# Optimization experiments

Measured on AMD Instinct MI355X. Metric: run time of the kernel, lower is better.

The kernel has to match this reference:

```python
import jax, jax.numpy as jnp
import numpy as np

B, T, D = 1, 2048, 2048
NH, NKV, HD = 16, 4, 128
REP = NH // NKV
ROPE_BASE = 10000.0


def rms_norm(x):
    # matches F.rms_norm default eps = finfo(dtype).eps
    eps = jnp.asarray(jnp.finfo(x.dtype).eps, x.dtype)
    return x * jax.lax.rsqrt(jnp.mean(x * x, axis=-1, keepdims=True) + eps)


def apply_rope(x, cos, sin):
    h = x.shape[-1] // 2
    x1, x2 = x[..., :h], x[..., h:]
    return jnp.concatenate([x1 * cos + x2 * sin, -x1 * sin + x2 * cos], axis=-1)


def setup_inputs() -> dict:
    key = jax.random.key(0)
    ks = jax.random.split(key, 9)
    s = 0.02  # weight init scale
    return {
        "x": jax.random.normal(ks[0], (B, T, D), jnp.float32),
        "skip": jax.random.normal(ks[1], (B, T, D), jnp.float32),
        "wq": jax.random.normal(ks[2], (D, D), jnp.float32) * s,
        "wk": jax.random.normal(ks[3], (NKV * HD, D), jnp.float32) * s,
        "wv": jax.random.normal(ks[4], (NKV * HD, D), jnp.float32) * s,
        "wproj": jax.random.normal(ks[5], (D, D), jnp.float32) * s,
        "qk_g": jnp.ones((NH,), jnp.float32),  # qk_init**0.5 with qk_init=1.0
        "ln_s": jnp.ones((1,), jnp.float32),
        "v_bias": jax.random.normal(ks[6], (NKV, HD), jnp.float32) * 0.01,
    }


def reference(x, skip, wq, wk, wv, wproj, qk_g, ln_s, v_bias):
    Bc, Tc, Dc = x.shape
    q = (x @ wq.T).reshape(Bc, Tc, NH, HD)        # [B,T,NH,HD]
    k = (x @ wk.T).reshape(Bc, Tc, NKV, HD)       # [B,T,NKV,HD]
    v = (x @ wv.T).reshape(Bc, Tc, NKV, HD) + v_bias[None, None, :, :]

    # skip-gate blend
    g = jax.nn.sigmoid(ln_s * 0.1)                # [1]
    ks_ = (skip @ wk.T).reshape(Bc, Tc, NKV, HD)
    vs_ = (skip @ wv.T).reshape(Bc, Tc, NKV, HD)
    k = k * (1.0 - g) + ks_ * g
    v = v * (1.0 - g) + vs_ * g

    q = rms_norm(q)
    k = rms_norm(k)

    # RoPE tables: [1, T, 1, HD/2]
    t = jnp.arange(Tc, dtype=jnp.float32)
    inv_freq = 1.0 / (ROPE_BASE ** (jnp.arange(0, HD, 2, dtype=jnp.float32) / HD))
    fr = t[:, None] * inv_freq[None, :]
    cos = jnp.cos(fr)[None, :, None, :].astype(x.dtype)
    sin = jnp.sin(fr)[None, :, None, :].astype(x.dtype)
    q = apply_rope(q, cos, sin)
    k = apply_rope(k, cos, sin)

    # per-head gain on q and on repeated k (effective gain^2 on logits)
    gain = jnp.abs(qk_g).astype(x.dtype)          # [NH]
    q = q * gain[None, None, :, None]
    k = jnp.repeat(k, REP, axis=2) * gain[None, None, :, None]  # [B,T,NH,HD]
    v = jnp.repeat(v, REP, axis=2)                               # [B,T,NH,HD]

    scale = 1.0 / jnp.sqrt(jnp.asarray(HD, x.dtype))
    scores = jnp.einsum('bqhd,bkhd->bhqk', q, k) * scale         # [B,NH,T,T]
    causal = jnp.tril(jnp.ones((Tc, Tc), dtype=bool))
    scores = jnp.where(causal[None, None], scores, -jnp.inf)
    attn = jax.nn.softmax(scores, axis=-1)
    y = jnp.einsum('bhqk,bkhd->bqhd', attn, v).reshape(Bc, Tc, Dc)
    return (y @ wproj.T) * ln_s.astype(x.dtype)
```

## Files before the change

### kernel.cpp

```cpp
#include <hip/hip_runtime.h>


typedef float  f32x4 __attribute__((ext_vector_type(4)));
typedef short  s16x8 __attribute__((ext_vector_type(8)));
typedef unsigned short u16;

#define DEVI __device__ __forceinline__

DEVI u16 f2bf(float f) {
  union { float f; unsigned u; } c; c.f = f;
  unsigned u = c.u + 0x7fffu + ((c.u >> 16) & 1u);
  return (u16)(u >> 16);
}

DEVI void gl_lds16(const void* g, void* l) {
  __builtin_amdgcn_global_load_lds(
      (const __attribute__((address_space(1))) unsigned int*)g,
      (__attribute__((address_space(3))) unsigned int*)l, 16, 0, 0);
}

__global__ __launch_bounds__(256) void prep_kernel(
    const float* __restrict__ x, const float* __restrict__ skip,
    const float* __restrict__ ln_s, const float* __restrict__ v_bias,
    u16* __restrict__ xb, u16* __restrict__ xmb, float* __restrict__ colbias) {
  float g = 1.0f / (1.0f + __expf(-ln_s[0] * 0.1f));
  int i = (blockIdx.x * 256 + threadIdx.x) * 4;
  float4 xv = *(const float4*)(x + i);
  float4 sv = *(const float4*)(skip + i);
  ushort4 a, b;
  a.x = f2bf(xv.x); a.y = f2bf(xv.y); a.z = f2bf(xv.z); a.w = f2bf(xv.w);
  b.x = f2bf((1.f - g) * xv.x + g * sv.x);
  b.y = f2bf((1.f - g) * xv.y + g * sv.y);
  b.z = f2bf((1.f - g) * xv.z + g * sv.z);
  b.w = f2bf((1.f - g) * xv.w + g * sv.w);
  *(ushort4*)(xb + i) = a;
  *(ushort4*)(xmb + i) = b;
  if (blockIdx.x == 0) {
    int t = threadIdx.x;
    for (int k = t; k < 512; k += 256) {
      colbias[k] = 0.f;
      colbias[512 + k] = (1.f - g) * v_bias[k];
    }
  }
}

__global__ __launch_bounds__(256) void convw_kernel(
    const float* __restrict__ wq, const float* __restrict__ wk,
    const float* __restrict__ wv, const float* __restrict__ wp,
    u16* __restrict__ wb) {
  size_t i = ((size_t)blockIdx.x * 256 + threadIdx.x) * 4;
  constexpr size_t M4 = 4u * 1024 * 1024, M1 = 1024 * 1024;
  const float* src;
  if (i < M4) src = wq + i;
  else if (i < M4 + M1) src = wk + (i - M4);
  else if (i < M4 + 2 * M1) src = wv + (i - M4 - M1);
  else src = wp + (i - M4 - 2 * M1);
  float4 v = *(const float4*)src;
  ushort4 o;
  o.x = f2bf(v.x); o.y = f2bf(v.y); o.z = f2bf(v.z); o.w = f2bf(v.w);
  *(ushort4*)(wb + i) = o;
}

template <int BIAS, int SCALE>
__global__ __launch_bounds__(256) void gemm_nt(
    const u16* __restrict__ A, const u16* __restrict__ B, float* __restrict__ C,
    int M, int N, int K, const float* __restrict__ bias,
    const float* __restrict__ scale) {
  __shared__ u16 lA[128 * 32];
  __shared__ u16 lB[128 * 32];
  const int tid = threadIdx.x;
  const int lane = tid & 63, w = tid >> 6;
  const int m0 = blockIdx.y * 128, n0 = blockIdx.x * 128;
  const int mo = (w >> 1) * 64, no = (w & 1) * 64;
  const int r16 = lane & 15, q4 = lane >> 4;
  f32x4 acc[4][4] = {};

  for (int k0 = 0; k0 < K; k0 += 32) {
#pragma unroll
    for (int j = 0; j < 2; ++j) {
      int slot = j * 256 + tid;
      int row = slot >> 2, c8 = (slot & 3) * 8;
      gl_lds16(A + (size_t)(m0 + row) * K + k0 + c8, &lA[slot * 8]);
    }
#pragma unroll
    for (int j = 0; j < 2; ++j) {
      int slot = j * 256 + tid;
      int row = slot >> 2, c8 = (slot & 3) * 8;
      gl_lds16(B + (size_t)(n0 + row) * K + k0 + c8, &lB[slot * 8]);
    }
    __syncthreads();
    s16x8 af[4], bfr[4];
#pragma unroll
    for (int i = 0; i < 4; ++i)
      af[i] = *(const s16x8*)&lA[(mo + i * 16 + r16) * 32 + q4 * 8];
#pragma unroll
    for (int i = 0; i < 4; ++i)
      bfr[i] = *(const s16x8*)&lB[(no + i * 16 + r16) * 32 + q4 * 8];
#pragma unroll
    for (int mi = 0; mi < 4; ++mi)
#pragma unroll
      for (int ni = 0; ni < 4; ++ni)
        acc[mi][ni] = __builtin_amdgcn_mfma_f32_16x16x32_bf16(
            af[mi], bfr[ni], acc[mi][ni], 0, 0, 0);
    __syncthreads();
  }
  float sc = SCALE ? scale[0] : 1.0f;
#pragma unroll
  for (int mi = 0; mi < 4; ++mi) {
#pragma unroll
    for (int ni = 0; ni < 4; ++ni) {
      int col = n0 + no + ni * 16 + r16;
      float bv = BIAS ? bias[col] : 0.0f;
#pragma unroll
      for (int r = 0; r < 4; ++r) {
        int row = m0 + mo + mi * 16 + q4 * 4 + r;
        C[(size_t)row * N + col] = (acc[mi][ni][r] + bv) * sc;
      }
    }
  }
}

__global__ __launch_bounds__(256) void postqk_kernel(
    const float* __restrict__ qraw, const float* __restrict__ kvraw,
    const float* __restrict__ qk_g, u16* __restrict__ qb,
    u16* __restrict__ kb) {
  constexpr int T = 2048;
  const int lane = threadIdx.x & 63, w = threadIdx.x >> 6;
  int p = blockIdx.x * 4 + w;
  const float* src;
  u16* dst;
  int t;
  float extra = 1.0f;
  if (p < 16 * T) {
    int hh = p >> 11; t = p & 2047;
    src = qraw + (size_t)t * 2048 + hh * 128;
    dst = qb + ((size_t)hh * T + t) * 128;
    float g = qk_g[hh];
    extra = g * g * 0.12751742f;
  } else {
    p -= 16 * T;
    int hh = p >> 11; t = p & 2047;
    src = kvraw + (size_t)t * 1024 + hh * 128;
    dst = kb + ((size_t)hh * T + t) * 128;
  }
  float x1 = src[lane], x2 = src[lane + 64];
  float ss = x1 * x1 + x2 * x2;
  ss += __shfl_xor(ss, 1);  ss += __shfl_xor(ss, 2);  ss += __shfl_xor(ss, 4);
  ss += __shfl_xor(ss, 8);  ss += __shfl_xor(ss, 16); ss += __shfl_xor(ss, 32);
  float rn = rsqrtf(ss * (1.0f / 128.0f) + 1.1920929e-7f) * extra;
  float fr = (float)t * expf((float)lane * -0.14391156831212787f);
  float c = cosf(fr), s = sinf(fr);
  float y1 = (x1 * c + x2 * s) * rn;
  float y2 = (x2 * c - x1 * s) * rn;
  dst[lane] = f2bf(y1);
  dst[lane + 64] = f2bf(y2);
}

__global__ __launch_bounds__(256) void transv_kernel(
    const float* __restrict__ kvraw, u16* __restrict__ vT) {
  constexpr int T = 2048;
  __shared__ float tile[32][33];
  int t0 = blockIdx.x * 32, hd0 = blockIdx.y * 32;
  int tx = threadIdx.x & 31, ty = threadIdx.x >> 5;
#pragma unroll
  for (int i = 0; i < 4; ++i) {
    int t = t0 + ty + i * 8;
    tile[ty + i * 8][tx] = kvraw[(size_t)t * 1024 + 512 + hd0 + tx];
  }
  __syncthreads();
#pragma unroll
  for (int i = 0; i < 4; ++i) {
    int hd = hd0 + ty + i * 8;
    vT[(size_t)hd * T + t0 + tx] = f2bf(tile[tx][ty + i * 8]);
  }
}

__global__ __launch_bounds__(256) void flash_kernel(
    const u16* __restrict__ qb, const u16* __restrict__ kb,
    const u16* __restrict__ vT, u16* __restrict__ out) {
  constexpr int T = 2048;
  __shared__ u16 lK[2][64 * 128];
  __shared__ u16 lV[2][128 * 64];
  __shared__ u16 lP[4][16 * 72];
  const int tid = threadIdx.x, lane = tid & 63, w = tid >> 6;
  const int h = blockIdx.y, hkv = h >> 2;
  const int q0 = (int)(gridDim.x - 1 - blockIdx.x) * 64;
  const int r16 = lane & 15, q4 = lane >> 4;
  const int qrow = q0 + w * 16 + q4 * 4;

  s16x8 qf[4];
  {
    const u16* qp = qb + ((size_t)h * T + q0 + w * 16 + r16) * 128 + q4 * 8;
#pragma unroll
    for (int d = 0; d < 4; ++d) qf[d] = *(const s16x8*)(qp + d * 32);
  }

  const u16* kbase = kb + (size_t)hkv * T * 128;
  const u16* vbase = vT + (size_t)hkv * 128 * T;
  int ks_off[4], vs_off[4];
#pragma unroll
  for (int j = 0; j < 4; ++j) {
    int slot = j * 256 + tid;
    int krow = slot >> 4, kc = slot & 15;
    int kcb = (kc * 16) ^ ((krow & 7) << 4);
    ks_off[j] = krow * 128 + (kcb >> 1);
    int vrow = slot >> 3, vc = slot & 7;
    int vcb = (vc * 16) ^ ((vrow & 7) << 4);
    vs_off[j] = vrow * T + (vcb >> 1);
  }

  f32x4 O[8] = {};
  float m_[4], l_[4];
#pragma unroll
  for (int r = 0; r < 4; ++r) { m_[r] = -3.0e38f; l_[r] = 0.f; }
  const int nt = q0 / 64 + 1;

#pragma unroll
  for (int j = 0; j < 4; ++j)
    gl_lds16(kbase + ks_off[j], &lK[0][(j * 256 + tid) * 8]);
#pragma unroll
  for (int j = 0; j < 4; ++j)
    gl_lds16(vbase + vs_off[j], &lV[0][(j * 256 + tid) * 8]);
  asm volatile("s_waitcnt vmcnt(0)" ::: "memory");
  __builtin_amdgcn_s_barrier();

  for (int it = 0; it < nt; ++it) {
    const int t0 = it * 64;
    const int cur = it & 1;
    if (it + 1 < nt) {
      const int nxt = (it + 1) * 64;
#pragma unroll
      for (int j = 0; j < 4; ++j)
        gl_lds16(kbase + (size_t)nxt * 128 + ks_off[j],
                 &lK[cur ^ 1][(j * 256 + tid) * 8]);
#pragma unroll
      for (int j = 0; j < 4; ++j)
        gl_lds16(vbase + nxt + vs_off[j],
                 &lV[cur ^ 1][(j * 256 + tid) * 8]);
    }
    const u16* Kt = lK[cur];
    const u16* Vt = lV[cur];

    f32x4 s[4];
#pragma unroll
    for (int kvh = 0; kvh < 4; ++kvh) {
      f32x4 acc = {};
#pragma unroll
      for (int d = 0; d < 4; ++d) {
        int cb = ((q4 * 16 + d * 64) ^ ((r16 & 7) << 4)) >> 1;
        acc = __builtin_amdgcn_mfma_f32_16x16x32_bf16(
            qf[d], *(const s16x8*)(Kt + (kvh * 16 + r16) * 128 + cb), acc, 0, 0, 0);
      }
      s[kvh] = acc;
    }

    if (t0 + 64 > q0 + w * 16) {
#pragma unroll
      for (int kvh = 0; kvh < 4; ++kvh)
#pragma unroll
        for (int r = 0; r < 4; ++r)
          s[kvh][r] = (t0 + kvh * 16 + r16 <= qrow + r) ? s[kvh][r] : -1.0e30f;
    }

    float al[4];
#pragma unroll
    for (int r = 0; r < 4; ++r) {
      float t = fmaxf(fmaxf(s[0][r], s[1][r]), fmaxf(s[2][r], s[3][r]));
      t = fmaxf(t, __shfl_xor(t, 1));
      t = fmaxf(t, __shfl_xor(t, 2));
      t = fmaxf(t, __shfl_xor(t, 4));
      t = fmaxf(t, __shfl_xor(t, 8));
      float mn = fmaxf(m_[r], t);
      al[r] = __builtin_amdgcn_exp2f(m_[r] - mn);
      m_[r] = mn;
    }
    u16* myP = lP[w];
#pragma unroll
    for (int r = 0; r < 4; ++r) {
      float ps = 0.f;
      int prow = (q4 * 4 + r) * 72;
#pragma unroll
      for (int kvh = 0; kvh < 4; ++kvh) {
        float pp = __builtin_amdgcn_exp2f(s[kvh][r] - m_[r]);
        myP[prow + kvh * 16 + r16] = f2bf(pp);
        ps += pp;
      }
      ps += __shfl_xor(ps, 1); ps += __shfl_xor(ps, 2);
      ps += __shfl_xor(ps, 4); ps += __shfl_xor(ps, 8);
      l_[r] = l_[r] * al[r] + ps;
    }
#pragma unroll
    for (int dt = 0; dt < 8; ++dt)
#pragma unroll
      for (int r = 0; r < 4; ++r) O[dt][r] *= al[r];

    asm volatile("s_waitcnt lgkmcnt(0)" ::: "memory");
    __builtin_amdgcn_sched_barrier(0);
    s16x8 pf0 = *(const s16x8*)&myP[r16 * 72 + q4 * 8];
    s16x8 pf1 = *(const s16x8*)&myP[r16 * 72 + 32 + q4 * 8];

    int cb0 = ((q4 * 16) ^ ((r16 & 7) << 4)) >> 1;
    int cb1 = ((64 + q4 * 16) ^ ((r16 & 7) << 4)) >> 1;
#pragma unroll
    for (int dt = 0; dt < 8; ++dt) {
      const u16* vr = Vt + (dt * 16 + r16) * 64;
      O[dt] = __builtin_amdgcn_mfma_f32_16x16x32_bf16(
          pf0, *(const s16x8*)(vr + cb0), O[dt], 0, 0, 0);
      O[dt] = __builtin_amdgcn_mfma_f32_16x16x32_bf16(
          pf1, *(const s16x8*)(vr + cb1), O[dt], 0, 0, 0);
    }

    asm volatile("s_waitcnt vmcnt(0)" ::: "memory");
    __builtin_amdgcn_s_barrier();
  }

  float inv[4];
#pragma unroll
  for (int r = 0; r < 4; ++r) inv[r] = 1.0f / l_[r];
#pragma unroll
  for (int dt = 0; dt < 8; ++dt) {
#pragma unroll
    for (int r = 0; r < 4; ++r) {
      int row = qrow + r;
      int col = h * 128 + dt * 16 + r16;
      out[(size_t)row * 2048 + col] = f2bf(O[dt][r] * inv[r]);
    }
  }
}

extern "C" void kernel_launch(void* const* d_in, const int* in_sizes, int n_in,
                              void* d_out, int out_size, void* d_ws,
                              size_t ws_size, hipStream_t stream) {
  const float* x      = (const float*)d_in[0];
  const float* skip   = (const float*)d_in[1];
  const float* wq     = (const float*)d_in[2];
  const float* wk     = (const float*)d_in[3];
  const float* wv     = (const float*)d_in[4];
  const float* wp     = (const float*)d_in[5];
  const float* qk_g   = (const float*)d_in[6];
  const float* ln_s   = (const float*)d_in[7];
  const float* v_bias = (const float*)d_in[8];
  float* out = (float*)d_out;

  constexpr size_t MB = 1024 * 1024;
  char* ws = (char*)d_ws;
  u16*   wb    = (u16*)(ws);
  u16*   xb    = (u16*)(ws + 20 * MB);
  u16*   xmb   = (u16*)(ws + 28 * MB);
  float* qraw  = (float*)(ws + 36 * MB);
  float* kvraw = (float*)(ws + 52 * MB);
  u16*   qb    = (u16*)(ws + 60 * MB);
  u16*   kb    = (u16*)(ws + 68 * MB);
  u16*   vT    = (u16*)(ws + 70 * MB);
  u16*   ao    = (u16*)(ws + 72 * MB);
  float* colbias = (float*)(ws + 80 * MB);

  prep_kernel<<<4096, 256, 0, stream>>>(x, skip, ln_s, v_bias, xb, xmb,
                                        colbias);
  convw_kernel<<<10240, 256, 0, stream>>>(wq, wk, wv, wp, wb);
  gemm_nt<0, 0><<<dim3(16, 16), 256, 0, stream>>>(xb, wb, qraw, 2048, 2048,
                                                  2048, nullptr, nullptr);
  gemm_nt<1, 0><<<dim3(8, 16), 256, 0, stream>>>(
      xmb, wb + 4 * MB, kvraw, 2048, 1024, 2048, colbias, nullptr);
  postqk_kernel<<<10240, 256, 0, stream>>>(qraw, kvraw, qk_g, qb, kb);
  transv_kernel<<<dim3(64, 16), 256, 0, stream>>>(kvraw, vT);
  flash_kernel<<<dim3(32, 16), 256, 0, stream>>>(qb, kb, vT, ao);
  gemm_nt<0, 1><<<dim3(16, 16), 256, 0, stream>>>(
      ao, wb + 6 * MB, out, 2048, 2048, 2048, nullptr, ln_s);
}
```

Measured before the change: 354.7 us.

## Split-K GEMMs with bf16 partials and single-wave flash blocks reading K/V from global

The three GEMMs now split K across blockIdx.z and write bf16 partial sums. The consumers (postqk, transv, and a new reduce_out kernel) add the partials back together, and the reduce kernel also applies the ln_s scale. This raises block counts on a GPU with many CUs. The flash kernel becomes one wave per block (16 query rows) and loads K and V straight from global memory instead of double-buffering them through LDS, so there are far more blocks but no shared K/V reuse. Storing partials in bf16 loses some precision, and the extra reduction pass adds memory traffic.

```diff
diff --git a/kernel.cpp b/kernel.cpp
--- a/kernel.cpp
+++ b/kernel.cpp
@@ -11,6 +11,10 @@
   union { float f; unsigned u; } c; c.f = f;
   unsigned u = c.u + 0x7fffu + ((c.u >> 16) & 1u);
   return (u16)(u >> 16);
+}
+DEVI float bf2f(u16 v) {
+  union { unsigned u; float f; } c; c.u = ((unsigned)v) << 16;
+  return c.f;
 }
 
 DEVI void gl_lds16(const void* g, void* l) {
@@ -61,21 +65,22 @@
   *(ushort4*)(wb + i) = o;
 }
 
-template <int BIAS, int SCALE>
-__global__ __launch_bounds__(256) void gemm_nt(
-    const u16* __restrict__ A, const u16* __restrict__ B, float* __restrict__ C,
-    int M, int N, int K, const float* __restrict__ bias,
-    const float* __restrict__ scale) {
+template <int BIAS>
+__global__ __launch_bounds__(256) void gemm_sk(
+    const u16* __restrict__ A, const u16* __restrict__ B, u16* __restrict__ Cp,
+    int M, int N, int KS, int K, const float* __restrict__ bias) {
   __shared__ u16 lA[128 * 32];
   __shared__ u16 lB[128 * 32];
   const int tid = threadIdx.x;
   const int lane = tid & 63, w = tid >> 6;
   const int m0 = blockIdx.y * 128, n0 = blockIdx.x * 128;
+  const int z = blockIdx.z;
   const int mo = (w >> 1) * 64, no = (w & 1) * 64;
   const int r16 = lane & 15, q4 = lane >> 4;
+  const int kbeg = z * KS;
   f32x4 acc[4][4] = {};
 
-  for (int k0 = 0; k0 < K; k0 += 32) {
+  for (int k0 = kbeg; k0 < kbeg + KS; k0 += 32) {
 #pragma unroll
     for (int j = 0; j < 2; ++j) {
       int slot = j * 256 + tid;
@@ -104,46 +109,52 @@
             af[mi], bfr[ni], acc[mi][ni], 0, 0, 0);
     __syncthreads();
   }
-  float sc = SCALE ? scale[0] : 1.0f;
+  u16* Cz = Cp + (size_t)z * M * N;
 #pragma unroll
   for (int mi = 0; mi < 4; ++mi) {
 #pragma unroll
     for (int ni = 0; ni < 4; ++ni) {
       int col = n0 + no + ni * 16 + r16;
-      float bv = BIAS ? bias[col] : 0.0f;
+      float bv = (BIAS && z == 0) ? bias[col] : 0.0f;
 #pragma unroll
       for (int r = 0; r < 4; ++r) {
         int row = m0 + mo + mi * 16 + q4 * 4 + r;
-        C[(size_t)row * N + col] = (acc[mi][ni][r] + bv) * sc;
+        Cz[(size_t)row * N + col] = f2bf(acc[mi][ni][r] + bv);
       }
     }
   }
 }
 
 __global__ __launch_bounds__(256) void postqk_kernel(
-    const float* __restrict__ qraw, const float* __restrict__ kvraw,
+    const u16* __restrict__ qrawp, const u16* __restrict__ kvrawp,
     const float* __restrict__ qk_g, u16* __restrict__ qb,
     u16* __restrict__ kb) {
   constexpr int T = 2048;
+  constexpr size_t QPS = (size_t)T * 2048;
+  constexpr size_t KPS = (size_t)T * 1024;
   const int lane = threadIdx.x & 63, w = threadIdx.x >> 6;
   int p = blockIdx.x * 4 + w;
-  const float* src;
   u16* dst;
   int t;
-  float extra = 1.0f;
+  float x1, x2, extra = 1.0f;
   if (p < 16 * T) {
     int hh = p >> 11; t = p & 2047;
-    src = qraw + (size_t)t * 2048 + hh * 128;
+    const u16* s0 = qrawp + (size_t)t * 2048 + hh * 128;
+    x1 = bf2f(s0[lane]) + bf2f(s0[QPS + lane]);
+    x2 = bf2f(s0[lane + 64]) + bf2f(s0[QPS + lane + 64]);
     dst = qb + ((size_t)hh * T + t) * 128;
     float g = qk_g[hh];
     extra = g * g * 0.12751742f;
   } else {
     p -= 16 * T;
     int hh = p >> 11; t = p & 2047;
-    src = kvraw + (size_t)t * 1024 + hh * 128;
+    const u16* s0 = kvrawp + (size_t)t * 1024 + hh * 128;
+    x1 = bf2f(s0[lane]) + bf2f(s0[KPS + lane]) + bf2f(s0[2 * KPS + lane]) +
+         bf2f(s0[3 * KPS + lane]);
+    x2 = bf2f(s0[lane + 64]) + bf2f(s0[KPS + lane + 64]) +
+         bf2f(s0[2 * KPS + lane + 64]) + bf2f(s0[3 * KPS + lane + 64]);
     dst = kb + ((size_t)hh * T + t) * 128;
   }
-  float x1 = src[lane], x2 = src[lane + 64];
   float ss = x1 * x1 + x2 * x2;
   ss += __shfl_xor(ss, 1);  ss += __shfl_xor(ss, 2);  ss += __shfl_xor(ss, 4);
   ss += __shfl_xor(ss, 8);  ss += __shfl_xor(ss, 16); ss += __shfl_xor(ss, 32);
@@ -157,15 +168,18 @@
 }
 
 __global__ __launch_bounds__(256) void transv_kernel(
-    const float* __restrict__ kvraw, u16* __restrict__ vT) {
+    const u16* __restrict__ kvrawp, u16* __restrict__ vT) {
   constexpr int T = 2048;
+  constexpr size_t KPS = (size_t)T * 1024;
   __shared__ float tile[32][33];
   int t0 = blockIdx.x * 32, hd0 = blockIdx.y * 32;
   int tx = threadIdx.x & 31, ty = threadIdx.x >> 5;
 #pragma unroll
   for (int i = 0; i < 4; ++i) {
     int t = t0 + ty + i * 8;
-    tile[ty + i * 8][tx] = kvraw[(size_t)t * 1024 + 512 + hd0 + tx];
+    const u16* s0 = kvrawp + (size_t)t * 1024 + 512 + hd0 + tx;
+    tile[ty + i * 8][tx] =
+        bf2f(s0[0]) + bf2f(s0[KPS]) + bf2f(s0[2 * KPS]) + bf2f(s0[3 * KPS]);
   }
   __syncthreads();
 #pragma unroll
@@ -175,93 +189,60 @@
   }
 }
 
-__global__ __launch_bounds__(256) void flash_kernel(
+__global__ __launch_bounds__(64) void flash_kernel(
     const u16* __restrict__ qb, const u16* __restrict__ kb,
     const u16* __restrict__ vT, u16* __restrict__ out) {
   constexpr int T = 2048;
-  __shared__ u16 lK[2][64 * 128];
-  __shared__ u16 lV[2][128 * 64];
-  __shared__ u16 lP[4][16 * 72];
-  const int tid = threadIdx.x, lane = tid & 63, w = tid >> 6;
+  __shared__ u16 lP[16 * 72];
+  const int lane = threadIdx.x;
   const int h = blockIdx.y, hkv = h >> 2;
-  const int q0 = (int)(gridDim.x - 1 - blockIdx.x) * 64;
+  const int qt = (int)(gridDim.x - 1 - blockIdx.x);
+  const int q0w = qt * 16;
   const int r16 = lane & 15, q4 = lane >> 4;
-  const int qrow = q0 + w * 16 + q4 * 4;
+  const int qrow = q0w + q4 * 4;
 
   s16x8 qf[4];
   {
-    const u16* qp = qb + ((size_t)h * T + q0 + w * 16 + r16) * 128 + q4 * 8;
+    const u16* qp = qb + ((size_t)h * T + q0w + r16) * 128 + q4 * 8;
 #pragma unroll
     for (int d = 0; d < 4; ++d) qf[d] = *(const s16x8*)(qp + d * 32);
   }
-
   const u16* kbase = kb + (size_t)hkv * T * 128;
   const u16* vbase = vT + (size_t)hkv * 128 * T;
-  int ks_off[4], vs_off[4];
-#pragma unroll
-  for (int j = 0; j < 4; ++j) {
-    int slot = j * 256 + tid;
-    int krow = slot >> 4, kc = slot & 15;
-    int kcb = (kc * 16) ^ ((krow & 7) << 4);
-    ks_off[j] = krow * 128 + (kcb >> 1);
-    int vrow = slot >> 3, vc = slot & 7;
-    int vcb = (vc * 16) ^ ((vrow & 7) << 4);
-    vs_off[j] = vrow * T + (vcb >> 1);
-  }
 
   f32x4 O[8] = {};
   float m_[4], l_[4];
 #pragma unroll
   for (int r = 0; r < 4; ++r) { m_[r] = -3.0e38f; l_[r] = 0.f; }
-  const int nt = q0 / 64 + 1;
-
-#pragma unroll
-  for (int j = 0; j < 4; ++j)
-    gl_lds16(kbase + ks_off[j], &lK[0][(j * 256 + tid) * 8]);
-#pragma unroll
-  for (int j = 0; j < 4; ++j)
-    gl_lds16(vbase + vs_off[j], &lV[0][(j * 256 + tid) * 8]);
-  asm volatile("s_waitcnt vmcnt(0)" ::: "memory");
-  __builtin_amdgcn_s_barrier();
+  const int nt = q0w / 64 + 1;
 
   for (int it = 0; it < nt; ++it) {
     const int t0 = it * 64;
-    const int cur = it & 1;
-    if (it + 1 < nt) {
-      const int nxt = (it + 1) * 64;
-#pragma unroll
-      for (int j = 0; j < 4; ++j)
-        gl_lds16(kbase + (size_t)nxt * 128 + ks_off[j],
-                 &lK[cur ^ 1][(j * 256 + tid) * 8]);
-#pragma unroll
-      for (int j = 0; j < 4; ++j)
-        gl_lds16(vbase + nxt + vs_off[j],
-                 &lV[cur ^ 1][(j * 256 + tid) * 8]);
-    }
-    const u16* Kt = lK[cur];
-    const u16* Vt = lV[cur];
-
     f32x4 s[4];
+    const u16* kt = kbase + (size_t)t0 * 128 + q4 * 8;
 #pragma unroll
     for (int kvh = 0; kvh < 4; ++kvh) {
+      const u16* kr = kt + (kvh * 16 + r16) * 128;
       f32x4 acc = {};
-#pragma unroll
-      for (int d = 0; d < 4; ++d) {
-        int cb = ((q4 * 16 + d * 64) ^ ((r16 & 7) << 4)) >> 1;
-        acc = __builtin_amdgcn_mfma_f32_16x16x32_bf16(
-            qf[d], *(const s16x8*)(Kt + (kvh * 16 + r16) * 128 + cb), acc, 0, 0, 0);
-      }
+      acc = __builtin_amdgcn_mfma_f32_16x16x32_bf16(qf[0], *(const s16x8*)(kr), acc, 0, 0, 0);
+      acc = __builtin_amdgcn_mfma_f32_16x16x32_bf16(qf[1], *(const s16x8*)(kr + 32), acc, 0, 0, 0);
+      acc = __builtin_amdgcn_mfma_f32_16x16x32_bf16(qf[2], *(const s16x8*)(kr + 64), acc, 0, 0, 0);
+      acc = __builtin_amdgcn_mfma_f32_16x16x32_bf16(qf[3], *(const s16x8*)(kr + 96), acc, 0, 0, 0);
       s[kvh] = acc;
     }
-
-    if (t0 + 64 > q0 + w * 16) {
+    const u16* vt = vbase + t0 + q4 * 8;
+    s16x8 vf[8];
+#pragma unroll
+    for (int dt = 0; dt < 8; ++dt)
+      vf[dt] = *(const s16x8*)(vt + (size_t)(dt * 16 + r16) * T);
+
+    if (t0 + 64 > q0w) {
 #pragma unroll
       for (int kvh = 0; kvh < 4; ++kvh)
 #pragma unroll
         for (int r = 0; r < 4; ++r)
           s[kvh][r] = (t0 + kvh * 16 + r16 <= qrow + r) ? s[kvh][r] : -1.0e30f;
     }
-
     float al[4];
 #pragma unroll
     for (int r = 0; r < 4; ++r) {
@@ -274,7 +255,6 @@
       al[r] = __builtin_amdgcn_exp2f(m_[r] - mn);
       m_[r] = mn;
     }
-    u16* myP = lP[w];
 #pragma unroll
     for (int r = 0; r < 4; ++r) {
       float ps = 0.f;
@@ -282,7 +262,7 @@
 #pragma unroll
       for (int kvh = 0; kvh < 4; ++kvh) {
         float pp = __builtin_amdgcn_exp2f(s[kvh][r] - m_[r]);
-        myP[prow + kvh * 16 + r16] = f2bf(pp);
+        lP[prow + kvh * 16 + r16] = f2bf(pp);
         ps += pp;
       }
       ps += __shfl_xor(ps, 1); ps += __shfl_xor(ps, 2);
@@ -296,22 +276,18 @@
 
     asm volatile("s_waitcnt lgkmcnt(0)" ::: "memory");
     __builtin_amdgcn_sched_barrier(0);
-    s16x8 pf0 = *(const s16x8*)&myP[r16 * 72 + q4 * 8];
-    s16x8 pf1 = *(const s16x8*)&myP[r16 * 72 + 32 + q4 * 8];
-
-    int cb0 = ((q4 * 16) ^ ((r16 & 7) << 4)) >> 1;
-    int cb1 = ((64 + q4 * 16) ^ ((r16 & 7) << 4)) >> 1;
-#pragma unroll
-    for (int dt = 0; dt < 8; ++dt) {
-      const u16* vr = Vt + (dt * 16 + r16) * 64;
-      O[dt] = __builtin_amdgcn_mfma_f32_16x16x32_bf16(
-          pf0, *(const s16x8*)(vr + cb0), O[dt], 0, 0, 0);
-      O[dt] = __builtin_amdgcn_mfma_f32_16x16x32_bf16(
-          pf1, *(const s16x8*)(vr + cb1), O[dt], 0, 0, 0);
-    }
-
-    asm volatile("s_waitcnt vmcnt(0)" ::: "memory");
-    __builtin_amdgcn_s_barrier();
+    s16x8 pf0 = *(const s16x8*)&lP[r16 * 72 + q4 * 8];
+    s16x8 pf1 = *(const s16x8*)&lP[r16 * 72 + 32 + q4 * 8];
+
+#pragma unroll
+    for (int dt = 0; dt < 8; ++dt)
+      O[dt] = __builtin_amdgcn_mfma_f32_16x16x32_bf16(pf0, vf[dt], O[dt], 0, 0, 0);
+#pragma unroll
+    for (int dt = 0; dt < 8; ++dt)
+      vf[dt] = *(const s16x8*)(vt + 32 + (size_t)(dt * 16 + r16) * T);
+#pragma unroll
+    for (int dt = 0; dt < 8; ++dt)
+      O[dt] = __builtin_amdgcn_mfma_f32_16x16x32_bf16(pf1, vf[dt], O[dt], 0, 0, 0);
   }
 
   float inv[4];
@@ -326,6 +302,22 @@
       out[(size_t)row * 2048 + col] = f2bf(O[dt][r] * inv[r]);
     }
   }
+}
+
+__global__ __launch_bounds__(256) void reduce_out_kernel(
+    const u16* __restrict__ p, const float* __restrict__ ln_s,
+    float* __restrict__ out) {
+  constexpr size_t PS = (size_t)2048 * 2048;
+  float sc = ln_s[0];
+  size_t i = ((size_t)blockIdx.x * 256 + threadIdx.x) * 4;
+  ushort4 a = *(const ushort4*)(p + i);
+  ushort4 b = *(const ushort4*)(p + PS + i);
+  float4 o;
+  o.x = (bf2f(a.x) + bf2f(b.x)) * sc;
+  o.y = (bf2f(a.y) + bf2f(b.y)) * sc;
+  o.z = (bf2f(a.z) + bf2f(b.z)) * sc;
+  o.w = (bf2f(a.w) + bf2f(b.w)) * sc;
+  *(float4*)(out + i) = o;
 }
 
 extern "C" void kernel_launch(void* const* d_in, const int* in_sizes, int n_in,
@@ -344,27 +336,29 @@
 
   constexpr size_t MB = 1024 * 1024;
   char* ws = (char*)d_ws;
-  u16*   wb    = (u16*)(ws);
-  u16*   xb    = (u16*)(ws + 20 * MB);
-  u16*   xmb   = (u16*)(ws + 28 * MB);
-  float* qraw  = (float*)(ws + 36 * MB);
-  float* kvraw = (float*)(ws + 52 * MB);
-  u16*   qb    = (u16*)(ws + 60 * MB);
-  u16*   kb    = (u16*)(ws + 68 * MB);
-  u16*   vT    = (u16*)(ws + 70 * MB);
-  u16*   ao    = (u16*)(ws + 72 * MB);
+  u16*   wb     = (u16*)(ws);
+  u16*   xb     = (u16*)(ws + 20 * MB);
+  u16*   xmb    = (u16*)(ws + 28 * MB);
+  u16*   qrawp  = (u16*)(ws + 36 * MB);
+  u16*   kvrawp = (u16*)(ws + 52 * MB);
+  u16*   qb     = (u16*)(ws + 68 * MB);
+  u16*   kb     = (u16*)(ws + 76 * MB);
+  u16*   vT     = (u16*)(ws + 78 * MB);
   float* colbias = (float*)(ws + 80 * MB);
+  u16*   ao     = xb;
+  u16*   outp   = qrawp;
 
   prep_kernel<<<4096, 256, 0, stream>>>(x, skip, ln_s, v_bias, xb, xmb,
                                         colbias);
   convw_kernel<<<10240, 256, 0, stream>>>(wq, wk, wv, wp, wb);
-  gemm_nt<0, 0><<<dim3(16, 16), 256, 0, stream>>>(xb, wb, qraw, 2048, 2048,
-                                                  2048, nullptr, nullptr);
-  gemm_nt<1, 0><<<dim3(8, 16), 256, 0, stream>>>(
-      xmb, wb + 4 * MB, kvraw, 2048, 1024, 2048, colbias, nullptr);
-  postqk_kernel<<<10240, 256, 0, stream>>>(qraw, kvraw, qk_g, qb, kb);
-  transv_kernel<<<dim3(64, 16), 256, 0, stream>>>(kvraw, vT);
-  flash_kernel<<<dim3(32, 16), 256, 0, stream>>>(qb, kb, vT, ao);
-  gemm_nt<0, 1><<<dim3(16, 16), 256, 0, stream>>>(
-      ao, wb + 6 * MB, out, 2048, 2048, 2048, nullptr, ln_s);
-}
+  gemm_sk<0><<<dim3(16, 16, 2), 256, 0, stream>>>(
+      xb, wb, qrawp, 2048, 2048, 1024, 2048, nullptr);
+  gemm_sk<1><<<dim3(8, 16, 4), 256, 0, stream>>>(
+      xmb, wb + 4 * MB, kvrawp, 2048, 1024, 512, 2048, colbias);
+  postqk_kernel<<<10240, 256, 0, stream>>>(qrawp, kvrawp, qk_g, qb, kb);
+  transv_kernel<<<dim3(64, 16), 256, 0, stream>>>(kvrawp, vT);
+  flash_kernel<<<dim3(128, 16), 64, 0, stream>>>(qb, kb, vT, ao);
+  gemm_sk<0><<<dim3(16, 16, 2), 256, 0, stream>>>(
+      ao, wb + 6 * MB, outp, 2048, 2048, 1024, 2048, nullptr);
+  reduce_out_kernel<<<4096, 256, 0, stream>>>(outp, ln_s, out);
+}
```

Result: slower. 471.0 us (+32.8%).
